# Optimization experiments

Hardware: AMD Instinct MI355X
Metric: run time of the kernel (lower is better)

Reference implementation:

```python
import jax, jax.numpy as jnp
import numpy as np

D_MODEL = 1024
ADAPT = 128
NUM_LIB = 8
BATCH = 1024


def setup_inputs() -> dict:
    key = jax.random.key(0)
    k_x, k_src, k_tgt, k_w1, k_w2 = jax.random.split(key, 5)
    hidden_states = jax.random.normal(k_x, (BATCH, D_MODEL), dtype=jnp.float32)
    source_library = jax.random.randint(k_src, (BATCH,), 0, NUM_LIB, dtype=jnp.int32)
    target_library = jax.random.randint(k_tgt, (BATCH,), 0, NUM_LIB, dtype=jnp.int32)
    # Stacked translator weights: slot p = src*NUM_LIB + tgt. Diagonal slots
    # (src==tgt) exist for uniform indexing but are masked out (identity path).
    P = NUM_LIB * NUM_LIB
    s1 = 1.0 / np.sqrt(D_MODEL).astype(np.float32)
    s2 = 1.0 / np.sqrt(ADAPT).astype(np.float32)
    W1 = jax.random.normal(k_w1, (P, D_MODEL, ADAPT), dtype=jnp.float32) * s1
    b1 = jnp.zeros((P, ADAPT), dtype=jnp.float32)
    W2 = jax.random.normal(k_w2, (P, ADAPT, D_MODEL), dtype=jnp.float32) * s2
    b2 = jnp.zeros((P, D_MODEL), dtype=jnp.float32)
    return {
        "hidden_states": hidden_states,
        "source_library": source_library,
        "target_library": target_library,
        "W1": W1, "b1": b1, "W2": W2, "b2": b2,
    }


def reference(hidden_states, source_library, target_library, W1, b1, W2, b2):
    # L recovered from stacked expert table [L*L, d, a]
    L = int(np.sqrt(W1.shape[0]))
    pair = source_library * L + target_library  # [B]
    # Per-sample expert weights (grouped-GEMM formulation of the python loop)
    h = jax.nn.relu(jnp.einsum('bd,bda->ba', hidden_states, W1[pair]) + b1[pair])
    y = jnp.einsum('ba,bad->bd', h, W2[pair]) + b2[pair]
    # src == tgt -> identity (original appends hidden_states[i] unchanged)
    same = (source_library == target_library)[:, None]
    return jnp.where(same, hidden_states, y)
```

## Files before the change

kernel.cpp:

```cpp
#include <hip/hip_runtime.h>
#include <hip/hip_bf16.h>

#define D_MODEL 1024
#define ADAPT   128
#define NUM_LIB 8
#define BATCH   1024
#define CH      32
#define NSLOT   96

typedef __attribute__((ext_vector_type(8))) short bf16x8;
typedef __attribute__((ext_vector_type(4))) float f32x4;

__device__ __forceinline__ unsigned pk2(float a, float b) {
  __hip_bfloat162 h = __float22bfloat162_rn(make_float2(a, b));
  return *(unsigned*)&h;
}

__global__ __launch_bounds__(1024) void bucket_k(const int* __restrict__ src,
                                                 const int* __restrict__ tgt,
                                                 int* __restrict__ perm,
                                                 int* __restrict__ cpair,
                                                 int* __restrict__ cbase,
                                                 int* __restrict__ cm) {
  __shared__ int cnt[64];
  __shared__ int offs[64];
  __shared__ int pos[64];
  __shared__ int choff[65];
  int t = threadIdx.x;
  if (t < 64) { cnt[t] = 0; pos[t] = 0; }
  __syncthreads();
  int pair = src[t] * NUM_LIB + tgt[t];
  atomicAdd(&cnt[pair], 1);
  __syncthreads();
  if (t == 0) {
    int acc = 0, ch = 0;
    for (int i = 0; i < 64; i++) {
      offs[i] = acc; acc += cnt[i];
      choff[i] = ch; ch += (cnt[i] + CH - 1) / CH;
    }
    choff[64] = ch;
  }
  __syncthreads();
  int sl = atomicAdd(&pos[pair], 1);
  perm[offs[pair] + sl] = t;
  if (t < 64) {
    int nc = (cnt[t] + CH - 1) / CH, c0 = choff[t];
    for (int c = 0; c < nc; c++) {
      cpair[c0 + c] = t;
      cbase[c0 + c] = offs[t] + c * CH;
      cm[c0 + c]    = min(CH, cnt[t] - c * CH);
    }
  } else if (t < 64 + NSLOT) {
    int slotid = t - 64;
    if (slotid >= choff[64]) cpair[slotid] = -1;
  }
}

#define BK     256
#define XS_STR 520
#define WT_STR 264

__global__ __launch_bounds__(256) void gemm1_k(const float* __restrict__ x,
                                               const float* __restrict__ W1,
                                               const int* __restrict__ perm,
                                               const int* __restrict__ cpair,
                                               const int* __restrict__ cbase,
                                               const int* __restrict__ cm,
                                               float* __restrict__ Hp) {
  int slot = blockIdx.x;
  int p = cpair[slot];
  if (p < 0 || (p % 9) == 0) return;
  int m    = cm[slot];
  int base = cbase[slot];
  int a0   = blockIdx.y * 64;
  int kh   = blockIdx.z;
  __shared__ int   rows_s[CH];
  __shared__ short xs[CH * XS_STR];
  __shared__ short wt[64 * WT_STR];
  int t = threadIdx.x;
  if (t < CH) rows_s[t] = perm[base + min(t, m - 1)];
  __syncthreads();
  {
    int s = t & 31, jg = t >> 5;
    const float* xr = x + (size_t)rows_s[s] * D_MODEL + kh * 512 + jg * 64;
    uint4* xw = (uint4*)(xs + s * XS_STR + jg * 64);
#pragma unroll
    for (int i = 0; i < 8; i++) {
      float4 v0 = *(const float4*)(xr + i * 8);
      float4 v1 = *(const float4*)(xr + i * 8 + 4);
      uint4 o;
      o.x = pk2(v0.x, v0.y); o.y = pk2(v0.z, v0.w);
      o.z = pk2(v1.x, v1.y); o.w = pk2(v1.z, v1.w);
      xw[i] = o;
    }
  }
  int lane = t & 63, wvid = t >> 6, col = lane & 15, quad = lane >> 4;
  f32x4 acc0 = {0.f, 0.f, 0.f, 0.f};
  f32x4 acc1 = {0.f, 0.f, 0.f, 0.f};
  int a_st = t & 63, kg = t >> 6;
  for (int r = 0; r < 2; r++) {
    {
      const float* wr = W1 + ((size_t)p * D_MODEL + kh * 512 + r * BK + kg * 64) * ADAPT + a0 + a_st;
      uint4* ww = (uint4*)(wt + a_st * WT_STR + kg * 64);
#pragma unroll
      for (int j8 = 0; j8 < 8; j8++) {
        uint4 o;
        o.x = pk2(wr[(j8 * 8 + 0) * ADAPT], wr[(j8 * 8 + 1) * ADAPT]);
        o.y = pk2(wr[(j8 * 8 + 2) * ADAPT], wr[(j8 * 8 + 3) * ADAPT]);
        o.z = pk2(wr[(j8 * 8 + 4) * ADAPT], wr[(j8 * 8 + 5) * ADAPT]);
        o.w = pk2(wr[(j8 * 8 + 6) * ADAPT], wr[(j8 * 8 + 7) * ADAPT]);
        ww[j8] = o;
      }
    }
    __syncthreads();
#pragma unroll
    for (int kk = 0; kk < 8; kk++) {
      bf16x8 af0 = *(const bf16x8*)(xs + col * XS_STR + r * BK + kk * 32 + quad * 8);
      bf16x8 af1 = *(const bf16x8*)(xs + (16 + col) * XS_STR + r * BK + kk * 32 + quad * 8);
      bf16x8 bv  = *(const bf16x8*)(wt + (wvid * 16 + col) * WT_STR + kk * 32 + quad * 8);
      acc0 = __builtin_amdgcn_mfma_f32_16x16x32_bf16(af0, bv, acc0, 0, 0, 0);
      acc1 = __builtin_amdgcn_mfma_f32_16x16x32_bf16(af1, bv, acc1, 0, 0, 0);
    }
    __syncthreads();
  }
  int a = a0 + wvid * 16 + col;
  float* Hb = Hp + (size_t)kh * BATCH * ADAPT;
#pragma unroll
  for (int r = 0; r < 4; r++) {
    int s = quad * 4 + r;
    if (s < m)      Hb[(size_t)rows_s[s] * ADAPT + a]      = acc0[r];
    if (s + 16 < m) Hb[(size_t)rows_s[s + 16] * ADAPT + a] = acc1[r];
  }
}

#define HS_STR  136
#define WT2_STR 136

__global__ __launch_bounds__(256) void gemm2_k(const float* __restrict__ x,
                                               const float* __restrict__ W2,
                                               const float* __restrict__ b1,
                                               const float* __restrict__ b2,
                                               const int* __restrict__ perm,
                                               const int* __restrict__ cpair,
                                               const int* __restrict__ cbase,
                                               const int* __restrict__ cm,
                                               const float* __restrict__ Hp,
                                               float* __restrict__ out) {
  int slot = blockIdx.x;
  int p = cpair[slot];
  if (p < 0) return;
  int m    = cm[slot];
  int base = cbase[slot];
  int d0   = blockIdx.y * 128;
  __shared__ int rows_s[CH];
  int t = threadIdx.x;
  if (t < CH) rows_s[t] = perm[base + min(t, m - 1)];
  __syncthreads();
  if ((p % 9) == 0) {
    int s = t >> 3, j = t & 7;
    if (s < m) {
      size_t off = (size_t)rows_s[s] * D_MODEL + d0 + j * 16;
      float4 v0 = *(const float4*)(x + off);
      float4 v1 = *(const float4*)(x + off + 4);
      float4 v2 = *(const float4*)(x + off + 8);
      float4 v3 = *(const float4*)(x + off + 12);
      *(float4*)(out + off)      = v0;
      *(float4*)(out + off + 4)  = v1;
      *(float4*)(out + off + 8)  = v2;
      *(float4*)(out + off + 12) = v3;
    }
    return;
  }
  __shared__ short hs[CH * HS_STR];
  __shared__ short wt[128 * WT2_STR];
  {
    int s = t & 31, j = t >> 5;
    size_t ho = (size_t)rows_s[s] * ADAPT + j * 16;
    const float* h0 = Hp + ho;
    const float* h1 = Hp + (size_t)BATCH * ADAPT + ho;
    const float* bb = b1 + (size_t)p * ADAPT + j * 16;
    uint4* hw = (uint4*)(hs + s * HS_STR + j * 16);
#pragma unroll
    for (int g = 0; g < 2; g++) {
      float v[8];
#pragma unroll
      for (int i = 0; i < 8; i++) v[i] = fmaxf(h0[g * 8 + i] + h1[g * 8 + i] + bb[g * 8 + i], 0.f);
      uint4 o;
      o.x = pk2(v[0], v[1]); o.y = pk2(v[2], v[3]);
      o.z = pk2(v[4], v[5]); o.w = pk2(v[6], v[7]);
      hw[g] = o;
    }
  }
  {
    int dl = t & 127, half = t >> 7;
#pragma unroll
    for (int kgi = 0; kgi < 8; kgi++) {
      int kb = kgi * 16 + half * 8;
      const float* wr = W2 + ((size_t)p * ADAPT + kb) * D_MODEL + d0 + dl;
      uint4 o;
      o.x = pk2(wr[0 * D_MODEL], wr[1 * D_MODEL]);
      o.y = pk2(wr[2 * D_MODEL], wr[3 * D_MODEL]);
      o.z = pk2(wr[4 * D_MODEL], wr[5 * D_MODEL]);
      o.w = pk2(wr[6 * D_MODEL], wr[7 * D_MODEL]);
      *(uint4*)(wt + dl * WT2_STR + kb) = o;
    }
  }
  __syncthreads();
  int lane = t & 63, wvid = t >> 6, col = lane & 15, quad = lane >> 4;
  f32x4 acc00 = {0.f, 0.f, 0.f, 0.f};
  f32x4 acc01 = {0.f, 0.f, 0.f, 0.f};
  f32x4 acc10 = {0.f, 0.f, 0.f, 0.f};
  f32x4 acc11 = {0.f, 0.f, 0.f, 0.f};
#pragma unroll
  for (int kk = 0; kk < 4; kk++) {
    bf16x8 af0 = *(const bf16x8*)(hs + col * HS_STR + kk * 32 + quad * 8);
    bf16x8 af1 = *(const bf16x8*)(hs + (16 + col) * HS_STR + kk * 32 + quad * 8);
    bf16x8 b0  = *(const bf16x8*)(wt + (wvid * 32 + col) * WT2_STR + kk * 32 + quad * 8);
    bf16x8 b1v = *(const bf16x8*)(wt + (wvid * 32 + 16 + col) * WT2_STR + kk * 32 + quad * 8);
    acc00 = __builtin_amdgcn_mfma_f32_16x16x32_bf16(af0, b0,  acc00, 0, 0, 0);
    acc01 = __builtin_amdgcn_mfma_f32_16x16x32_bf16(af0, b1v, acc01, 0, 0, 0);
    acc10 = __builtin_amdgcn_mfma_f32_16x16x32_bf16(af1, b0,  acc10, 0, 0, 0);
    acc11 = __builtin_amdgcn_mfma_f32_16x16x32_bf16(af1, b1v, acc11, 0, 0, 0);
  }
  int d_a = d0 + wvid * 32 + col;
  int d_b = d_a + 16;
  float bba = b2[(size_t)p * D_MODEL + d_a];
  float bbb = b2[(size_t)p * D_MODEL + d_b];
#pragma unroll
  for (int r = 0; r < 4; r++) {
    int s = quad * 4 + r;
    if (s < m) {
      size_t ro = (size_t)rows_s[s] * D_MODEL;
      out[ro + d_a] = acc00[r] + bba;
      out[ro + d_b] = acc01[r] + bbb;
    }
    if (s + 16 < m) {
      size_t ro = (size_t)rows_s[s + 16] * D_MODEL;
      out[ro + d_a] = acc10[r] + bba;
      out[ro + d_b] = acc11[r] + bbb;
    }
  }
}

extern "C" void kernel_launch(void* const* d_in, const int* in_sizes, int n_in,
                              void* d_out, int out_size, void* d_ws, size_t ws_size,
                              hipStream_t stream) {
  const float* x   = (const float*)d_in[0];
  const int*   src = (const int*)d_in[1];
  const int*   tgt = (const int*)d_in[2];
  const float* W1  = (const float*)d_in[3];
  const float* b1  = (const float*)d_in[4];
  const float* W2  = (const float*)d_in[5];
  const float* b2  = (const float*)d_in[6];
  float* out = (float*)d_out;

  float* Hp   = (float*)d_ws;
  int* perm   = (int*)(Hp + 2 * (size_t)BATCH * ADAPT);
  int* cpair  = perm + BATCH;
  int* cbase  = cpair + NSLOT;
  int* cmarr  = cbase + NSLOT;

  bucket_k<<<1, 1024, 0, stream>>>(src, tgt, perm, cpair, cbase, cmarr);
  gemm1_k<<<dim3(NSLOT, 2, 2), 256, 0, stream>>>(x, W1, perm, cpair, cbase, cmarr, Hp);
  gemm2_k<<<dim3(NSLOT, 8), 256, 0, stream>>>(x, W2, b1, b2, perm, cpair, cbase, cmarr, Hp, out);
  (void)in_sizes; (void)n_in; (void)out_size; (void)ws_size;
}
```

Baseline: 122.4 us.

## Split K four ways in gemm1, halve gemm2 tiles, parallelize bucket prefix scan

```diff
diff --git a/kernel.cpp b/kernel.cpp
--- a/kernel.cpp
+++ b/kernel.cpp
@@ -32,19 +32,26 @@
   int pair = src[t] * NUM_LIB + tgt[t];
   atomicAdd(&cnt[pair], 1);
   __syncthreads();
-  if (t == 0) {
-    int acc = 0, ch = 0;
-    for (int i = 0; i < 64; i++) {
-      offs[i] = acc; acc += cnt[i];
-      choff[i] = ch; ch += (cnt[i] + CH - 1) / CH;
-    }
-    choff[64] = ch;
+  if (t < 64) {
+    int c   = cnt[t];
+    int nch = (c + CH - 1) >> 5;
+    int v   = c | (nch << 16);
+    int incl = v;
+#pragma unroll
+    for (int off = 1; off < 64; off <<= 1) {
+      int u = __shfl_up(incl, off, 64);
+      if (t >= off) incl += u;
+    }
+    int excl = incl - v;
+    offs[t]  = excl & 0xFFFF;
+    choff[t] = excl >> 16;
+    if (t == 63) choff[64] = incl >> 16;
   }
   __syncthreads();
   int sl = atomicAdd(&pos[pair], 1);
   perm[offs[pair] + sl] = t;
   if (t < 64) {
-    int nc = (cnt[t] + CH - 1) / CH, c0 = choff[t];
+    int nc = (cnt[t] + CH - 1) >> 5, c0 = choff[t];
     for (int c = 0; c < nc; c++) {
       cpair[c0 + c] = t;
       cbase[c0 + c] = offs[t] + c * CH;
@@ -57,7 +64,7 @@
 }
 
 #define BK     256
-#define XS_STR 520
+#define XS_STR 264
 #define WT_STR 264
 
 __global__ __launch_bounds__(256) void gemm1_k(const float* __restrict__ x,
@@ -73,19 +80,19 @@
   int m    = cm[slot];
   int base = cbase[slot];
   int a0   = blockIdx.y * 64;
-  int kh   = blockIdx.z;
+  int k0   = blockIdx.z * BK;
   __shared__ int   rows_s[CH];
   __shared__ short xs[CH * XS_STR];
   __shared__ short wt[64 * WT_STR];
   int t = threadIdx.x;
+  int r_own = perm[base + min(t & 31, m - 1)];
   if (t < CH) rows_s[t] = perm[base + min(t, m - 1)];
-  __syncthreads();
   {
     int s = t & 31, jg = t >> 5;
-    const float* xr = x + (size_t)rows_s[s] * D_MODEL + kh * 512 + jg * 64;
-    uint4* xw = (uint4*)(xs + s * XS_STR + jg * 64);
-#pragma unroll
-    for (int i = 0; i < 8; i++) {
+    const float* xr = x + (size_t)r_own * D_MODEL + k0 + jg * 32;
+    uint4* xw = (uint4*)(xs + s * XS_STR + jg * 32);
+#pragma unroll
+    for (int i = 0; i < 4; i++) {
       float4 v0 = *(const float4*)(xr + i * 8);
       float4 v1 = *(const float4*)(xr + i * 8 + 4);
       uint4 o;
@@ -94,37 +101,34 @@
       xw[i] = o;
     }
   }
+  {
+    int a_st = t & 63, kg = t >> 6;
+    const float* wr = W1 + ((size_t)p * D_MODEL + k0 + kg * 64) * ADAPT + a0 + a_st;
+    uint4* ww = (uint4*)(wt + a_st * WT_STR + kg * 64);
+#pragma unroll
+    for (int j8 = 0; j8 < 8; j8++) {
+      uint4 o;
+      o.x = pk2(wr[(j8 * 8 + 0) * ADAPT], wr[(j8 * 8 + 1) * ADAPT]);
+      o.y = pk2(wr[(j8 * 8 + 2) * ADAPT], wr[(j8 * 8 + 3) * ADAPT]);
+      o.z = pk2(wr[(j8 * 8 + 4) * ADAPT], wr[(j8 * 8 + 5) * ADAPT]);
+      o.w = pk2(wr[(j8 * 8 + 6) * ADAPT], wr[(j8 * 8 + 7) * ADAPT]);
+      ww[j8] = o;
+    }
+  }
+  __syncthreads();
   int lane = t & 63, wvid = t >> 6, col = lane & 15, quad = lane >> 4;
   f32x4 acc0 = {0.f, 0.f, 0.f, 0.f};
   f32x4 acc1 = {0.f, 0.f, 0.f, 0.f};
-  int a_st = t & 63, kg = t >> 6;
-  for (int r = 0; r < 2; r++) {
-    {
-      const float* wr = W1 + ((size_t)p * D_MODEL + kh * 512 + r * BK + kg * 64) * ADAPT + a0 + a_st;
-      uint4* ww = (uint4*)(wt + a_st * WT_STR + kg * 64);
-#pragma unroll
-      for (int j8 = 0; j8 < 8; j8++) {
-        uint4 o;
-        o.x = pk2(wr[(j8 * 8 + 0) * ADAPT], wr[(j8 * 8 + 1) * ADAPT]);
-        o.y = pk2(wr[(j8 * 8 + 2) * ADAPT], wr[(j8 * 8 + 3) * ADAPT]);
-        o.z = pk2(wr[(j8 * 8 + 4) * ADAPT], wr[(j8 * 8 + 5) * ADAPT]);
-        o.w = pk2(wr[(j8 * 8 + 6) * ADAPT], wr[(j8 * 8 + 7) * ADAPT]);
-        ww[j8] = o;
-      }
-    }
-    __syncthreads();
-#pragma unroll
-    for (int kk = 0; kk < 8; kk++) {
-      bf16x8 af0 = *(const bf16x8*)(xs + col * XS_STR + r * BK + kk * 32 + quad * 8);
-      bf16x8 af1 = *(const bf16x8*)(xs + (16 + col) * XS_STR + r * BK + kk * 32 + quad * 8);
-      bf16x8 bv  = *(const bf16x8*)(wt + (wvid * 16 + col) * WT_STR + kk * 32 + quad * 8);
-      acc0 = __builtin_amdgcn_mfma_f32_16x16x32_bf16(af0, bv, acc0, 0, 0, 0);
-      acc1 = __builtin_amdgcn_mfma_f32_16x16x32_bf16(af1, bv, acc1, 0, 0, 0);
-    }
-    __syncthreads();
+#pragma unroll
+  for (int kk = 0; kk < 8; kk++) {
+    bf16x8 af0 = *(const bf16x8*)(xs + col * XS_STR + kk * 32 + quad * 8);
+    bf16x8 af1 = *(const bf16x8*)(xs + (16 + col) * XS_STR + kk * 32 + quad * 8);
+    bf16x8 bv  = *(const bf16x8*)(wt + (wvid * 16 + col) * WT_STR + kk * 32 + quad * 8);
+    acc0 = __builtin_amdgcn_mfma_f32_16x16x32_bf16(af0, bv, acc0, 0, 0, 0);
+    acc1 = __builtin_amdgcn_mfma_f32_16x16x32_bf16(af1, bv, acc1, 0, 0, 0);
   }
   int a = a0 + wvid * 16 + col;
-  float* Hb = Hp + (size_t)kh * BATCH * ADAPT;
+  float* Hb = Hp + (size_t)blockIdx.z * BATCH * ADAPT;
 #pragma unroll
   for (int r = 0; r < 4; r++) {
     int s = quad * 4 + r;
@@ -151,40 +155,41 @@
   if (p < 0) return;
   int m    = cm[slot];
   int base = cbase[slot];
-  int d0   = blockIdx.y * 128;
-  __shared__ int rows_s[CH];
+  int d0   = blockIdx.y * 64;
   int t = threadIdx.x;
-  if (t < CH) rows_s[t] = perm[base + min(t, m - 1)];
-  __syncthreads();
   if ((p % 9) == 0) {
     int s = t >> 3, j = t & 7;
+    int row = perm[base + min(s, m - 1)];
     if (s < m) {
-      size_t off = (size_t)rows_s[s] * D_MODEL + d0 + j * 16;
+      size_t off = (size_t)row * D_MODEL + d0 + j * 8;
       float4 v0 = *(const float4*)(x + off);
       float4 v1 = *(const float4*)(x + off + 4);
-      float4 v2 = *(const float4*)(x + off + 8);
-      float4 v3 = *(const float4*)(x + off + 12);
-      *(float4*)(out + off)      = v0;
-      *(float4*)(out + off + 4)  = v1;
-      *(float4*)(out + off + 8)  = v2;
-      *(float4*)(out + off + 12) = v3;
+      *(float4*)(out + off)     = v0;
+      *(float4*)(out + off + 4) = v1;
     }
     return;
   }
+  __shared__ int rows_s[CH];
   __shared__ short hs[CH * HS_STR];
-  __shared__ short wt[128 * WT2_STR];
+  __shared__ short wt[64 * WT2_STR];
+  int r_own = perm[base + min(t & 31, m - 1)];
+  if (t < CH) rows_s[t] = perm[base + min(t, m - 1)];
   {
     int s = t & 31, j = t >> 5;
-    size_t ho = (size_t)rows_s[s] * ADAPT + j * 16;
+    size_t ho = (size_t)r_own * ADAPT + j * 16;
     const float* h0 = Hp + ho;
-    const float* h1 = Hp + (size_t)BATCH * ADAPT + ho;
     const float* bb = b1 + (size_t)p * ADAPT + j * 16;
     uint4* hw = (uint4*)(hs + s * HS_STR + j * 16);
 #pragma unroll
     for (int g = 0; g < 2; g++) {
       float v[8];
 #pragma unroll
-      for (int i = 0; i < 8; i++) v[i] = fmaxf(h0[g * 8 + i] + h1[g * 8 + i] + bb[g * 8 + i], 0.f);
+      for (int i = 0; i < 8; i++) {
+        float acc = bb[g * 8 + i];
+#pragma unroll
+        for (int q = 0; q < 4; q++) acc += h0[(size_t)q * BATCH * ADAPT + g * 8 + i];
+        v[i] = fmaxf(acc, 0.f);
+      }
       uint4 o;
       o.x = pk2(v[0], v[1]); o.y = pk2(v[2], v[3]);
       o.z = pk2(v[4], v[5]); o.w = pk2(v[6], v[7]);
@@ -192,10 +197,10 @@
     }
   }
   {
-    int dl = t & 127, half = t >> 7;
-#pragma unroll
-    for (int kgi = 0; kgi < 8; kgi++) {
-      int kb = kgi * 16 + half * 8;
+    int dl = t & 63, kg = t >> 6;
+#pragma unroll
+    for (int j8 = 0; j8 < 4; j8++) {
+      int kb = kg * 32 + j8 * 8;
       const float* wr = W2 + ((size_t)p * ADAPT + kb) * D_MODEL + d0 + dl;
       uint4 o;
       o.x = pk2(wr[0 * D_MODEL], wr[1 * D_MODEL]);
@@ -207,38 +212,23 @@
   }
   __syncthreads();
   int lane = t & 63, wvid = t >> 6, col = lane & 15, quad = lane >> 4;
-  f32x4 acc00 = {0.f, 0.f, 0.f, 0.f};
-  f32x4 acc01 = {0.f, 0.f, 0.f, 0.f};
-  f32x4 acc10 = {0.f, 0.f, 0.f, 0.f};
-  f32x4 acc11 = {0.f, 0.f, 0.f, 0.f};
+  f32x4 acc0 = {0.f, 0.f, 0.f, 0.f};
+  f32x4 acc1 = {0.f, 0.f, 0.f, 0.f};
 #pragma unroll
   for (int kk = 0; kk < 4; kk++) {
     bf16x8 af0 = *(const bf16x8*)(hs + col * HS_STR + kk * 32 + quad * 8);
     bf16x8 af1 = *(const bf16x8*)(hs + (16 + col) * HS_STR + kk * 32 + quad * 8);
-    bf16x8 b0  = *(const bf16x8*)(wt + (wvid * 32 + col) * WT2_STR + kk * 32 + quad * 8);
-    bf16x8 b1v = *(const bf16x8*)(wt + (wvid * 32 + 16 + col) * WT2_STR + kk * 32 + quad * 8);
-    acc00 = __builtin_amdgcn_mfma_f32_16x16x32_bf16(af0, b0,  acc00, 0, 0, 0);
-    acc01 = __builtin_amdgcn_mfma_f32_16x16x32_bf16(af0, b1v, acc01, 0, 0, 0);
-    acc10 = __builtin_amdgcn_mfma_f32_16x16x32_bf16(af1, b0,  acc10, 0, 0, 0);
-    acc11 = __builtin_amdgcn_mfma_f32_16x16x32_bf16(af1, b1v, acc11, 0, 0, 0);
-  }
-  int d_a = d0 + wvid * 32 + col;
-  int d_b = d_a + 16;
+    bf16x8 bv  = *(const bf16x8*)(wt + (wvid * 16 + col) * WT2_STR + kk * 32 + quad * 8);
+    acc0 = __builtin_amdgcn_mfma_f32_16x16x32_bf16(af0, bv, acc0, 0, 0, 0);
+    acc1 = __builtin_amdgcn_mfma_f32_16x16x32_bf16(af1, bv, acc1, 0, 0, 0);
+  }
+  int d_a = d0 + wvid * 16 + col;
   float bba = b2[(size_t)p * D_MODEL + d_a];
-  float bbb = b2[(size_t)p * D_MODEL + d_b];
 #pragma unroll
   for (int r = 0; r < 4; r++) {
     int s = quad * 4 + r;
-    if (s < m) {
-      size_t ro = (size_t)rows_s[s] * D_MODEL;
-      out[ro + d_a] = acc00[r] + bba;
-      out[ro + d_b] = acc01[r] + bbb;
-    }
-    if (s + 16 < m) {
-      size_t ro = (size_t)rows_s[s + 16] * D_MODEL;
-      out[ro + d_a] = acc10[r] + bba;
-      out[ro + d_b] = acc11[r] + bbb;
-    }
+    if (s < m)      out[(size_t)rows_s[s] * D_MODEL + d_a]      = acc0[r] + bba;
+    if (s + 16 < m) out[(size_t)rows_s[s + 16] * D_MODEL + d_a] = acc1[r] + bba;
   }
 }
 
@@ -255,13 +245,13 @@
   float* out = (float*)d_out;
 
   float* Hp   = (float*)d_ws;
-  int* perm   = (int*)(Hp + 2 * (size_t)BATCH * ADAPT);
+  int* perm   = (int*)(Hp + 4 * (size_t)BATCH * ADAPT);
   int* cpair  = perm + BATCH;
   int* cbase  = cpair + NSLOT;
   int* cmarr  = cbase + NSLOT;
 
   bucket_k<<<1, 1024, 0, stream>>>(src, tgt, perm, cpair, cbase, cmarr);
-  gemm1_k<<<dim3(NSLOT, 2, 2), 256, 0, stream>>>(x, W1, perm, cpair, cbase, cmarr, Hp);
-  gemm2_k<<<dim3(NSLOT, 8), 256, 0, stream>>>(x, W2, b1, b2, perm, cpair, cbase, cmarr, Hp, out);
+  gemm1_k<<<dim3(NSLOT, 2, 4), 256, 0, stream>>>(x, W1, perm, cpair, cbase, cmarr, Hp);
+  gemm2_k<<<dim3(NSLOT, 16), 256, 0, stream>>>(x, W2, b1, b2, perm, cpair, cbase, cmarr, Hp, out);
   (void)in_sizes; (void)n_in; (void)out_size; (void)ws_size;
 }
```

Result: no change. 120.8 us (-1.3%).

## Drop bucketing kernel; each pair block gathers its own rows in-kernel

Applied to the files above, without the earlier changes.

```diff
diff --git a/kernel.cpp b/kernel.cpp
--- a/kernel.cpp
+++ b/kernel.cpp
@@ -6,7 +6,6 @@
 #define NUM_LIB 8
 #define BATCH   1024
 #define CH      32
-#define NSLOT   96
 
 typedef __attribute__((ext_vector_type(8))) short bf16x8;
 typedef __attribute__((ext_vector_type(4))) float f32x4;
@@ -16,120 +15,89 @@
   return *(unsigned*)&h;
 }
 
-__global__ __launch_bounds__(1024) void bucket_k(const int* __restrict__ src,
-                                                 const int* __restrict__ tgt,
-                                                 int* __restrict__ perm,
-                                                 int* __restrict__ cpair,
-                                                 int* __restrict__ cbase,
-                                                 int* __restrict__ cm) {
-  __shared__ int cnt[64];
-  __shared__ int offs[64];
-  __shared__ int pos[64];
-  __shared__ int choff[65];
-  int t = threadIdx.x;
-  if (t < 64) { cnt[t] = 0; pos[t] = 0; }
-  __syncthreads();
-  int pair = src[t] * NUM_LIB + tgt[t];
-  atomicAdd(&cnt[pair], 1);
-  __syncthreads();
-  if (t == 0) {
-    int acc = 0, ch = 0;
-    for (int i = 0; i < 64; i++) {
-      offs[i] = acc; acc += cnt[i];
-      choff[i] = ch; ch += (cnt[i] + CH - 1) / CH;
-    }
-    choff[64] = ch;
-  }
-  __syncthreads();
-  int sl = atomicAdd(&pos[pair], 1);
-  perm[offs[pair] + sl] = t;
-  if (t < 64) {
-    int nc = (cnt[t] + CH - 1) / CH, c0 = choff[t];
-    for (int c = 0; c < nc; c++) {
-      cpair[c0 + c] = t;
-      cbase[c0 + c] = offs[t] + c * CH;
-      cm[c0 + c]    = min(CH, cnt[t] - c * CH);
-    }
-  } else if (t < 64 + NSLOT) {
-    int slotid = t - 64;
-    if (slotid >= choff[64]) cpair[slotid] = -1;
-  }
-}
-
 #define BK     256
-#define XS_STR 520
+#define XS_STR 264
 #define WT_STR 264
 
 __global__ __launch_bounds__(256) void gemm1_k(const float* __restrict__ x,
                                                const float* __restrict__ W1,
-                                               const int* __restrict__ perm,
-                                               const int* __restrict__ cpair,
-                                               const int* __restrict__ cbase,
-                                               const int* __restrict__ cm,
+                                               const int* __restrict__ src,
+                                               const int* __restrict__ tgt,
                                                float* __restrict__ Hp) {
-  int slot = blockIdx.x;
-  int p = cpair[slot];
-  if (p < 0 || (p % 9) == 0) return;
-  int m    = cm[slot];
-  int base = cbase[slot];
-  int a0   = blockIdx.y * 64;
-  int kh   = blockIdx.z;
-  __shared__ int   rows_s[CH];
+  int p = blockIdx.x;
+  if ((p % 9) == 0) return;
+  int a0 = blockIdx.y * 64;
+  int k0 = blockIdx.z * BK;
+  __shared__ int   nrows;
+  __shared__ int   rows_l[BATCH];
   __shared__ short xs[CH * XS_STR];
   __shared__ short wt[64 * WT_STR];
   int t = threadIdx.x;
-  if (t < CH) rows_s[t] = perm[base + min(t, m - 1)];
-  __syncthreads();
-  {
-    int s = t & 31, jg = t >> 5;
-    const float* xr = x + (size_t)rows_s[s] * D_MODEL + kh * 512 + jg * 64;
-    uint4* xw = (uint4*)(xs + s * XS_STR + jg * 64);
-#pragma unroll
-    for (int i = 0; i < 8; i++) {
-      float4 v0 = *(const float4*)(xr + i * 8);
-      float4 v1 = *(const float4*)(xr + i * 8 + 4);
+  if (t == 0) nrows = 0;
+  __syncthreads();
+  {
+#pragma unroll
+    for (int i = 0; i < 4; i++) {
+      int s = t + 256 * i;
+      int pr = src[s] * NUM_LIB + tgt[s];
+      if (pr == p) rows_l[atomicAdd(&nrows, 1)] = s;
+    }
+  }
+  {
+    int a_st = t & 63, kg = t >> 6;
+    const float* wr = W1 + ((size_t)p * D_MODEL + k0 + kg * 64) * ADAPT + a0 + a_st;
+    uint4* ww = (uint4*)(wt + a_st * WT_STR + kg * 64);
+#pragma unroll
+    for (int j8 = 0; j8 < 8; j8++) {
       uint4 o;
-      o.x = pk2(v0.x, v0.y); o.y = pk2(v0.z, v0.w);
-      o.z = pk2(v1.x, v1.y); o.w = pk2(v1.z, v1.w);
-      xw[i] = o;
-    }
-  }
+      o.x = pk2(wr[(j8 * 8 + 0) * ADAPT], wr[(j8 * 8 + 1) * ADAPT]);
+      o.y = pk2(wr[(j8 * 8 + 2) * ADAPT], wr[(j8 * 8 + 3) * ADAPT]);
+      o.z = pk2(wr[(j8 * 8 + 4) * ADAPT], wr[(j8 * 8 + 5) * ADAPT]);
+      o.w = pk2(wr[(j8 * 8 + 6) * ADAPT], wr[(j8 * 8 + 7) * ADAPT]);
+      ww[j8] = o;
+    }
+  }
+  __syncthreads();
+  int n = nrows;
+  if (n == 0) return;
   int lane = t & 63, wvid = t >> 6, col = lane & 15, quad = lane >> 4;
-  f32x4 acc0 = {0.f, 0.f, 0.f, 0.f};
-  f32x4 acc1 = {0.f, 0.f, 0.f, 0.f};
-  int a_st = t & 63, kg = t >> 6;
-  for (int r = 0; r < 2; r++) {
+  float* Hb = Hp + (size_t)blockIdx.z * BATCH * ADAPT;
+  for (int c0 = 0; c0 < n; c0 += CH) {
+    int m = min(CH, n - c0);
     {
-      const float* wr = W1 + ((size_t)p * D_MODEL + kh * 512 + r * BK + kg * 64) * ADAPT + a0 + a_st;
-      uint4* ww = (uint4*)(wt + a_st * WT_STR + kg * 64);
-#pragma unroll
-      for (int j8 = 0; j8 < 8; j8++) {
+      int s = t & 31, jg = t >> 5;
+      int row = rows_l[c0 + min(s, m - 1)];
+      const float* xr = x + (size_t)row * D_MODEL + k0 + jg * 32;
+      uint4* xw = (uint4*)(xs + s * XS_STR + jg * 32);
+#pragma unroll
+      for (int i = 0; i < 4; i++) {
+        float4 v0 = *(const float4*)(xr + i * 8);
+        float4 v1 = *(const float4*)(xr + i * 8 + 4);
         uint4 o;
-        o.x = pk2(wr[(j8 * 8 + 0) * ADAPT], wr[(j8 * 8 + 1) * ADAPT]);
-        o.y = pk2(wr[(j8 * 8 + 2) * ADAPT], wr[(j8 * 8 + 3) * ADAPT]);
-        o.z = pk2(wr[(j8 * 8 + 4) * ADAPT], wr[(j8 * 8 + 5) * ADAPT]);
-        o.w = pk2(wr[(j8 * 8 + 6) * ADAPT], wr[(j8 * 8 + 7) * ADAPT]);
-        ww[j8] = o;
+        o.x = pk2(v0.x, v0.y); o.y = pk2(v0.z, v0.w);
+        o.z = pk2(v1.x, v1.y); o.w = pk2(v1.z, v1.w);
+        xw[i] = o;
       }
     }
     __syncthreads();
+    f32x4 acc0 = {0.f, 0.f, 0.f, 0.f};
+    f32x4 acc1 = {0.f, 0.f, 0.f, 0.f};
 #pragma unroll
     for (int kk = 0; kk < 8; kk++) {
-      bf16x8 af0 = *(const bf16x8*)(xs + col * XS_STR + r * BK + kk * 32 + quad * 8);
-      bf16x8 af1 = *(const bf16x8*)(xs + (16 + col) * XS_STR + r * BK + kk * 32 + quad * 8);
+      bf16x8 af0 = *(const bf16x8*)(xs + col * XS_STR + kk * 32 + quad * 8);
+      bf16x8 af1 = *(const bf16x8*)(xs + (16 + col) * XS_STR + kk * 32 + quad * 8);
       bf16x8 bv  = *(const bf16x8*)(wt + (wvid * 16 + col) * WT_STR + kk * 32 + quad * 8);
       acc0 = __builtin_amdgcn_mfma_f32_16x16x32_bf16(af0, bv, acc0, 0, 0, 0);
       acc1 = __builtin_amdgcn_mfma_f32_16x16x32_bf16(af1, bv, acc1, 0, 0, 0);
     }
-    __syncthreads();
-  }
-  int a = a0 + wvid * 16 + col;
-  float* Hb = Hp + (size_t)kh * BATCH * ADAPT;
-#pragma unroll
-  for (int r = 0; r < 4; r++) {
-    int s = quad * 4 + r;
-    if (s < m)      Hb[(size_t)rows_s[s] * ADAPT + a]      = acc0[r];
-    if (s + 16 < m) Hb[(size_t)rows_s[s + 16] * ADAPT + a] = acc1[r];
+    int a = a0 + wvid * 16 + col;
+#pragma unroll
+    for (int r = 0; r < 4; r++) {
+      int s2 = quad * 4 + r;
+      if (s2 < m)      Hb[(size_t)rows_l[c0 + s2] * ADAPT + a]      = acc0[r];
+      if (s2 + 16 < m) Hb[(size_t)rows_l[c0 + s2 + 16] * ADAPT + a] = acc1[r];
+    }
+    if (c0 + CH < n) __syncthreads();
   }
 }
 
@@ -140,26 +108,31 @@
                                                const float* __restrict__ W2,
                                                const float* __restrict__ b1,
                                                const float* __restrict__ b2,
-                                               const int* __restrict__ perm,
-                                               const int* __restrict__ cpair,
-                                               const int* __restrict__ cbase,
-                                               const int* __restrict__ cm,
+                                               const int* __restrict__ src,
+                                               const int* __restrict__ tgt,
                                                const float* __restrict__ Hp,
                                                float* __restrict__ out) {
-  int slot = blockIdx.x;
-  int p = cpair[slot];
-  if (p < 0) return;
-  int m    = cm[slot];
-  int base = cbase[slot];
-  int d0   = blockIdx.y * 128;
-  __shared__ int rows_s[CH];
+  int p = blockIdx.x;
+  int d0 = blockIdx.y * 128;
+  __shared__ int nrows;
+  __shared__ int rows_l[BATCH];
   int t = threadIdx.x;
-  if (t < CH) rows_s[t] = perm[base + min(t, m - 1)];
-  __syncthreads();
+  if (t == 0) nrows = 0;
+  __syncthreads();
+  {
+#pragma unroll
+    for (int i = 0; i < 4; i++) {
+      int s = t + 256 * i;
+      int pr = src[s] * NUM_LIB + tgt[s];
+      if (pr == p) rows_l[atomicAdd(&nrows, 1)] = s;
+    }
+  }
   if ((p % 9) == 0) {
-    int s = t >> 3, j = t & 7;
-    if (s < m) {
-      size_t off = (size_t)rows_s[s] * D_MODEL + d0 + j * 16;
+    __syncthreads();
+    int n = nrows;
+    int j = t & 7;
+    for (int c = t >> 3; c < n; c += 32) {
+      size_t off = (size_t)rows_l[c] * D_MODEL + d0 + j * 16;
       float4 v0 = *(const float4*)(x + off);
       float4 v1 = *(const float4*)(x + off + 4);
       float4 v2 = *(const float4*)(x + off + 8);
@@ -173,24 +146,6 @@
   }
   __shared__ short hs[CH * HS_STR];
   __shared__ short wt[128 * WT2_STR];
-  {
-    int s = t & 31, j = t >> 5;
-    size_t ho = (size_t)rows_s[s] * ADAPT + j * 16;
-    const float* h0 = Hp + ho;
-    const float* h1 = Hp + (size_t)BATCH * ADAPT + ho;
-    const float* bb = b1 + (size_t)p * ADAPT + j * 16;
-    uint4* hw = (uint4*)(hs + s * HS_STR + j * 16);
-#pragma unroll
-    for (int g = 0; g < 2; g++) {
-      float v[8];
-#pragma unroll
-      for (int i = 0; i < 8; i++) v[i] = fmaxf(h0[g * 8 + i] + h1[g * 8 + i] + bb[g * 8 + i], 0.f);
-      uint4 o;
-      o.x = pk2(v[0], v[1]); o.y = pk2(v[2], v[3]);
-      o.z = pk2(v[4], v[5]); o.w = pk2(v[6], v[7]);
-      hw[g] = o;
-    }
-  }
   {
     int dl = t & 127, half = t >> 7;
 #pragma unroll
@@ -206,39 +161,68 @@
     }
   }
   __syncthreads();
+  int n = nrows;
+  if (n == 0) return;
   int lane = t & 63, wvid = t >> 6, col = lane & 15, quad = lane >> 4;
-  f32x4 acc00 = {0.f, 0.f, 0.f, 0.f};
-  f32x4 acc01 = {0.f, 0.f, 0.f, 0.f};
-  f32x4 acc10 = {0.f, 0.f, 0.f, 0.f};
-  f32x4 acc11 = {0.f, 0.f, 0.f, 0.f};
-#pragma unroll
-  for (int kk = 0; kk < 4; kk++) {
-    bf16x8 af0 = *(const bf16x8*)(hs + col * HS_STR + kk * 32 + quad * 8);
-    bf16x8 af1 = *(const bf16x8*)(hs + (16 + col) * HS_STR + kk * 32 + quad * 8);
-    bf16x8 b0  = *(const bf16x8*)(wt + (wvid * 32 + col) * WT2_STR + kk * 32 + quad * 8);
-    bf16x8 b1v = *(const bf16x8*)(wt + (wvid * 32 + 16 + col) * WT2_STR + kk * 32 + quad * 8);
-    acc00 = __builtin_amdgcn_mfma_f32_16x16x32_bf16(af0, b0,  acc00, 0, 0, 0);
-    acc01 = __builtin_amdgcn_mfma_f32_16x16x32_bf16(af0, b1v, acc01, 0, 0, 0);
-    acc10 = __builtin_amdgcn_mfma_f32_16x16x32_bf16(af1, b0,  acc10, 0, 0, 0);
-    acc11 = __builtin_amdgcn_mfma_f32_16x16x32_bf16(af1, b1v, acc11, 0, 0, 0);
-  }
-  int d_a = d0 + wvid * 32 + col;
-  int d_b = d_a + 16;
-  float bba = b2[(size_t)p * D_MODEL + d_a];
-  float bbb = b2[(size_t)p * D_MODEL + d_b];
-#pragma unroll
-  for (int r = 0; r < 4; r++) {
-    int s = quad * 4 + r;
-    if (s < m) {
-      size_t ro = (size_t)rows_s[s] * D_MODEL;
-      out[ro + d_a] = acc00[r] + bba;
-      out[ro + d_b] = acc01[r] + bbb;
-    }
-    if (s + 16 < m) {
-      size_t ro = (size_t)rows_s[s + 16] * D_MODEL;
-      out[ro + d_a] = acc10[r] + bba;
-      out[ro + d_b] = acc11[r] + bbb;
-    }
+  for (int c0 = 0; c0 < n; c0 += CH) {
+    int m = min(CH, n - c0);
+    {
+      int s = t & 31, j = t >> 5;
+      int row = rows_l[c0 + min(s, m - 1)];
+      size_t ho = (size_t)row * ADAPT + j * 16;
+      const float* bb = b1 + (size_t)p * ADAPT + j * 16;
+      uint4* hw = (uint4*)(hs + s * HS_STR + j * 16);
+#pragma unroll
+      for (int g = 0; g < 2; g++) {
+        float v[8];
+#pragma unroll
+        for (int i = 0; i < 8; i++) {
+          float acc = bb[g * 8 + i];
+#pragma unroll
+          for (int q = 0; q < 4; q++) acc += Hp[(size_t)q * BATCH * ADAPT + ho + g * 8 + i];
+          v[i] = fmaxf(acc, 0.f);
+        }
+        uint4 o;
+        o.x = pk2(v[0], v[1]); o.y = pk2(v[2], v[3]);
+        o.z = pk2(v[4], v[5]); o.w = pk2(v[6], v[7]);
+        hw[g] = o;
+      }
+    }
+    __syncthreads();
+    f32x4 acc00 = {0.f, 0.f, 0.f, 0.f};
+    f32x4 acc01 = {0.f, 0.f, 0.f, 0.f};
+    f32x4 acc10 = {0.f, 0.f, 0.f, 0.f};
+    f32x4 acc11 = {0.f, 0.f, 0.f, 0.f};
+#pragma unroll
+    for (int kk = 0; kk < 4; kk++) {
+      bf16x8 af0 = *(const bf16x8*)(hs + col * HS_STR + kk * 32 + quad * 8);
+      bf16x8 af1 = *(const bf16x8*)(hs + (16 + col) * HS_STR + kk * 32 + quad * 8);
+      bf16x8 b0  = *(const bf16x8*)(wt + (wvid * 32 + col) * WT2_STR + kk * 32 + quad * 8);
+      bf16x8 b1v = *(const bf16x8*)(wt + (wvid * 32 + 16 + col) * WT2_STR + kk * 32 + quad * 8);
+      acc00 = __builtin_amdgcn_mfma_f32_16x16x32_bf16(af0, b0,  acc00, 0, 0, 0);
+      acc01 = __builtin_amdgcn_mfma_f32_16x16x32_bf16(af0, b1v, acc01, 0, 0, 0);
+      acc10 = __builtin_amdgcn_mfma_f32_16x16x32_bf16(af1, b0,  acc10, 0, 0, 0);
+      acc11 = __builtin_amdgcn_mfma_f32_16x16x32_bf16(af1, b1v, acc11, 0, 0, 0);
+    }
+    int d_a = d0 + wvid * 32 + col;
+    int d_b = d_a + 16;
+    float bba = b2[(size_t)p * D_MODEL + d_a];
+    float bbb = b2[(size_t)p * D_MODEL + d_b];
+#pragma unroll
+    for (int r = 0; r < 4; r++) {
+      int s2 = quad * 4 + r;
+      if (s2 < m) {
+        size_t ro = (size_t)rows_l[c0 + s2] * D_MODEL;
+        out[ro + d_a] = acc00[r] + bba;
+        out[ro + d_b] = acc01[r] + bbb;
+      }
+      if (s2 + 16 < m) {
+        size_t ro = (size_t)rows_l[c0 + s2 + 16] * D_MODEL;
+        out[ro + d_a] = acc10[r] + bba;
+        out[ro + d_b] = acc11[r] + bbb;
+      }
+    }
+    if (c0 + CH < n) __syncthreads();
   }
 }
 
@@ -254,14 +238,9 @@
   const float* b2  = (const float*)d_in[6];
   float* out = (float*)d_out;
 
-  float* Hp   = (float*)d_ws;
-  int* perm   = (int*)(Hp + 2 * (size_t)BATCH * ADAPT);
-  int* cpair  = perm + BATCH;
-  int* cbase  = cpair + NSLOT;
-  int* cmarr  = cbase + NSLOT;
-
-  bucket_k<<<1, 1024, 0, stream>>>(src, tgt, perm, cpair, cbase, cmarr);
-  gemm1_k<<<dim3(NSLOT, 2, 2), 256, 0, stream>>>(x, W1, perm, cpair, cbase, cmarr, Hp);
-  gemm2_k<<<dim3(NSLOT, 8), 256, 0, stream>>>(x, W2, b1, b2, perm, cpair, cbase, cmarr, Hp, out);
+  float* Hp = (float*)d_ws;
+
+  gemm1_k<<<dim3(64, 2, 4), 256, 0, stream>>>(x, W1, src, tgt, Hp);
+  gemm2_k<<<dim3(64, 8), 256, 0, stream>>>(x, W2, b1, b2, src, tgt, Hp, out);
   (void)in_sizes; (void)n_in; (void)out_size; (void)ws_size;
 }
```

After: 116.7 us (median of 2 runs). -4.6%, faster.
